# Kernel tuning notes

Hardware: AMD Instinct MI355X
Metric: run time of the kernel (lower is better)

Reference implementation:

```python
import jax, jax.numpy as jnp
import numpy as np

T, N, D, H = 128, 512, 1024, 1024
LN_EPS = 1e-5


def setup_inputs() -> dict:
    key = jax.random.key(0)
    ks = jax.random.split(key, 6)
    x = jax.random.normal(ks[0], (T * N, D), jnp.float32)
    hxs = jax.random.normal(ks[1], (N, 1, H), jnp.float32)
    # binary done-masks (float, mostly 1.0 = keep hidden state, 0.0 = episode reset)
    masks = (jax.random.uniform(ks[2], (T * N, 1)) < 0.95).astype(jnp.float32)
    s = 1.0 / np.sqrt(H)
    # PyTorch GRU packed gates, order (r, z, n): weight_ih_l0 [3H, D], weight_hh_l0 [3H, H]
    W_ih = jax.random.normal(ks[3], (3 * H, D), jnp.float32) * s
    W_hh = jax.random.normal(ks[4], (3 * H, H), jnp.float32) * s
    b_ih = jnp.zeros((3 * H,), jnp.float32)  # module inits biases to 0
    b_hh = jnp.zeros((3 * H,), jnp.float32)
    gamma = jnp.ones((H,), jnp.float32)
    beta = jnp.zeros((H,), jnp.float32)
    return dict(x=x, hxs=hxs, masks=masks, W_ih=W_ih, W_hh=W_hh,
                b_ih=b_ih, b_hh=b_hh, gamma=gamma, beta=beta)


def reference(x, hxs, masks, W_ih, W_hh, b_ih, b_hh, gamma, beta):
    TN = x.shape[0]
    Nn = hxs.shape[0]
    Tt = TN // Nn
    Hd = hxs.shape[-1]
    xs = x.reshape(Tt, Nn, -1)          # [T, N, D]
    m = masks.reshape(Tt, Nn)           # [T, N]
    # Chunk starts per source: t=0 plus every t>=1 where (masks[t] == 1).any().
    # At a chunk start the hidden state is multiplied by masks[t] (broadcast over layers);
    # a scan with a per-step conditional mask-multiply is exactly equivalent to the
    # torch loop over chunks.
    reset = jnp.concatenate([jnp.ones((1,), bool), jnp.any(m[1:] == 1.0, axis=-1)])
    # Batch the input projection across all T*N tokens (one big GEMM): [T, N, 3H]
    xp = jnp.einsum('tnd,gd->tng', xs, W_ih) + b_ih
    h0 = hxs[:, 0, :]                   # recurrent_N == 1 -> [N, H]

    def step(h, inp):
        xp_t, m_t, r_t = inp
        h = jnp.where(r_t, h * m_t[:, None], h)
        hp = h @ W_hh.T + b_hh          # [N, 3H]
        xr, xz, xn = jnp.split(xp_t, 3, axis=-1)
        hr, hz, hn = jnp.split(hp, 3, axis=-1)
        r = jax.nn.sigmoid(xr + hr)
        z = jax.nn.sigmoid(xz + hz)
        n = jnp.tanh(xn + r * hn)
        h_new = (1.0 - z) * n + z * h
        return h_new, h_new

    h_last, outs = jax.lax.scan(step, h0, (xp, m, reset))
    y = outs.reshape(Tt * Nn, Hd)
    # LayerNorm over last dim
    mu = y.mean(-1, keepdims=True)
    var = y.var(-1, keepdims=True)
    y = (y - mu) * jax.lax.rsqrt(var + LN_EPS) * gamma + beta
    return y, h_last[:, None, :]
```

## Files before the change

kernel.cpp:

```cpp
#include <hip/hip_runtime.h>

#define T_STEPS 128
#define N_B     512
#define D_IN    1024
#define H_DIM   1024
#define G_DIM   3072
#define M_ALL   (T_STEPS * N_B)
#define BAR_STRIDE 64

typedef short          s8v  __attribute__((ext_vector_type(8)));
typedef float          f4v  __attribute__((ext_vector_type(4)));
typedef unsigned short u4v  __attribute__((ext_vector_type(4)));

__device__ __forceinline__ unsigned short f2bf(float f) {
  union { float f; unsigned u; } v; v.f = f;
  unsigned r = v.u + 0x7FFFu + ((v.u >> 16) & 1u);
  return (unsigned short)(r >> 16);
}
__device__ __forceinline__ float bf2f(unsigned short h) {
  union { unsigned u; float f; } v; v.u = ((unsigned)h) << 16;
  return v.f;
}
__device__ __forceinline__ void async16(const void* g, void* l) {
  __builtin_amdgcn_global_load_lds(
      (const __attribute__((address_space(1))) unsigned*)g,
      (__attribute__((address_space(3))) unsigned*)l, 16, 0, 0);
}
__device__ __forceinline__ void async16_coh(const void* g, void* l) {
  __builtin_amdgcn_global_load_lds(
      (const __attribute__((address_space(1))) unsigned*)g,
      (__attribute__((address_space(3))) unsigned*)l, 16, 0, 17);
}
__device__ __forceinline__ void store_bf16_coh(unsigned short* p, unsigned short v) {
  unsigned v32 = v;
  asm volatile("global_store_short %0, %1, off sc0 sc1" :: "v"(p), "v"(v32) : "memory");
}
__device__ __forceinline__ float sigmoidf_(float x) { return 1.f / (1.f + __expf(-x)); }
__device__ __forceinline__ float tanhf_(float x)    { return 1.f - 2.f / (1.f + __expf(2.f * x)); }

__global__ void cvt_bf16(const float* __restrict__ in, unsigned short* __restrict__ out, long n4) {
  long i = (long)blockIdx.x * blockDim.x + threadIdx.x;
  long stride = (long)gridDim.x * blockDim.x;
  for (; i < n4; i += stride) {
    f4v v = *(const f4v*)(in + i * 4);
    u4v o;
    #pragma unroll
    for (int e = 0; e < 4; ++e) o[e] = f2bf(v[e]);
    *(u4v*)(out + i * 4) = o;
  }
}

__global__ void reset_kernel(const float* __restrict__ masks, int* __restrict__ reset) {
  const int t = blockIdx.x;
  __shared__ int flag;
  if (threadIdx.x == 0) flag = (t == 0) ? 1 : 0;
  __syncthreads();
  if (t > 0 && masks[(size_t)t * N_B + threadIdx.x] == 1.0f) flag = 1;
  __syncthreads();
  if (threadIdx.x == 0) reset[t] = flag;
}

__global__ __launch_bounds__(256) void gemm_xp(const unsigned short* __restrict__ A,
                                               const unsigned short* __restrict__ B,
                                               const float* __restrict__ bias,
                                               unsigned short* __restrict__ C) {
  const int m0 = blockIdx.y * 128, g0 = blockIdx.x * 128;
  const int tid = threadIdx.x, wv = tid >> 6, l = tid & 63;
  const int l15 = l & 15, l4 = l >> 4;
  const int wr = wv >> 1, wc = wv & 1;
  __shared__ unsigned short As[128 * 64], Bs[128 * 64];

  f4v zero4 = {0.f, 0.f, 0.f, 0.f};
  f4v acc[4][4];
  #pragma unroll
  for (int i = 0; i < 4; ++i)
    #pragma unroll
    for (int j = 0; j < 4; ++j) acc[i][j] = zero4;

  const int srow = l >> 3;
  const int selem = ((l & 7) ^ srow) * 8;
  const int swz_rd = (l15 & 7) << 4;

  for (int kt = 0; kt < 1024; kt += 64) {
    #pragma unroll
    for (int cc = 0; cc < 4; ++cc) {
      int s = wv * 4 + cc;
      int row = s * 8 + srow;
      async16(A + (size_t)(m0 + row) * 1024 + kt + selem, &As[s * 512]);
      async16(B + (size_t)(g0 + row) * 1024 + kt + selem, &Bs[s * 512]);
    }
    __syncthreads();
    #pragma unroll
    for (int ks = 0; ks < 2; ++ks) {
      s8v a[4], b[4];
      #pragma unroll
      for (int i = 0; i < 4; ++i) {
        int ra = wr * 64 + i * 16 + l15, rb = wc * 64 + i * 16 + l15;
        int cb = (ks * 64 + l4 * 16) ^ swz_rd;
        a[i] = *(const s8v*)((const char*)As + ra * 128 + cb);
        b[i] = *(const s8v*)((const char*)Bs + rb * 128 + cb);
      }
      #pragma unroll
      for (int i = 0; i < 4; ++i)
        #pragma unroll
        for (int j = 0; j < 4; ++j)
          acc[i][j] = __builtin_amdgcn_mfma_f32_16x16x32_bf16(a[i], b[j], acc[i][j], 0, 0, 0);
    }
    __syncthreads();
  }
  #pragma unroll
  for (int j = 0; j < 4; ++j) {
    int gcol = g0 + wc * 64 + j * 16 + l15;
    float bv = bias[gcol];
    #pragma unroll
    for (int i = 0; i < 4; ++i) {
      int mrow = m0 + wr * 64 + i * 16 + l4 * 4;
      u4v o;
      #pragma unroll
      for (int r = 0; r < 4; ++r) o[r] = f2bf(acc[i][j][r] + bv);
      *(u4v*)(C + (size_t)gcol * M_ALL + mrow) = o;
    }
  }
}

__global__ __launch_bounds__(256, 1) void rnn_all(
    const unsigned short* __restrict__ Whh,
    const unsigned short* __restrict__ xpT,
    const float* __restrict__ masks,
    const int* __restrict__ reset,
    const float* __restrict__ bhh,
    const float* __restrict__ hxs,
    unsigned short* hbuf,
    float* __restrict__ y,
    float* __restrict__ hlast,
    unsigned* bar) {
  const int bid = blockIdx.x;
  const int jt = bid & 31, nt = bid >> 5;
  const int j0 = jt * 32, n0 = nt * 64;
  const int tid = threadIdx.x, w = tid >> 6, l = tid & 63;
  const int l15 = l & 15, l4 = l >> 4;
  const int wn = w & 1, wj = w >> 1;
  const size_t NH = (size_t)N_B * H_DIM;

  __shared__ unsigned short Hs[3][64 * 128];
  __shared__ unsigned short Ws[3][96 * 128];
  __shared__ unsigned short xpl[3][32][64];

  const int lrow4 = l >> 4;
  const int lcb = (l & 15) * 16;
  const int swz_rd = (l15 & 7) << 4;

  const int jj = j0 + wj * 16 + l15;
  const float br = bhh[jj];
  const float bz = bhh[H_DIM + jj];
  const float bn = bhh[2 * H_DIM + jj];

  float hreg[2][4];
  #pragma unroll
  for (int i = 0; i < 2; ++i)
    #pragma unroll
    for (int r = 0; r < 4; ++r)
      hreg[i][r] = hxs[(size_t)(n0 + wn * 32 + i * 16 + l4 * 4 + r) * H_DIM + jj];

  f4v zero4 = {0.f, 0.f, 0.f, 0.f};
  s8v zer8 = {0, 0, 0, 0, 0, 0, 0, 0};

  auto stageH = [&](const unsigned short* hread, int buf, int kt) {
    #pragma unroll
    for (int q = 0; q < 4; ++q) {
      int rb = w * 16 + q * 4;
      int row = rb + lrow4;
      int cb = lcb ^ ((row & 7) << 4);
      async16_coh(hread + (size_t)(n0 + row) * H_DIM + kt * 128 + (cb >> 1),
                  &Hs[buf][rb * 128]);
    }
  };
  auto stageW = [&](int buf, int kt) {
    #pragma unroll
    for (int q = 0; q < 6; ++q) {
      int rb = w * 24 + q * 4;
      int row = rb + lrow4;
      int gate = row >> 5, jjl = row & 31;
      int cb = lcb ^ ((row & 7) << 4);
      async16(Whh + ((size_t)gate * H_DIM + j0 + jjl) * H_DIM + kt * 128 + (cb >> 1),
              &Ws[buf][rb * 128]);
    }
  };
  auto stageXP = [&](int t) {
    const int jl = w * 8 + (l >> 3);
    const int nelem = ((l & 7) ^ (l >> 3)) * 8;
    #pragma unroll
    for (int g3 = 0; g3 < 3; ++g3)
      async16(xpT + (size_t)(g3 * H_DIM + j0 + jl) * M_ALL + (size_t)t * N_B + n0 + nelem,
              &xpl[g3][w * 8][0]);
  };

  int rst = reset[0];
  bool zo[2];
  float mreg[2][4];
  #pragma unroll
  for (int i = 0; i < 2; ++i) {
    float mv = masks[(size_t)0 * N_B + n0 + wn * 32 + i * 16 + l15];
    zo[i] = rst && (mv == 0.0f);
  }
  #pragma unroll
  for (int i = 0; i < 2; ++i)
    #pragma unroll
    for (int r = 0; r < 4; ++r)
      mreg[i][r] = masks[(size_t)0 * N_B + n0 + wn * 32 + i * 16 + l4 * 4 + r];
  stageW(0, 0); stageW(1, 1); stageW(2, 2);
  stageXP(0);

  for (int t = 0; t < T_STEPS; ++t) {
    const unsigned short* hread = hbuf + (size_t)(t & 1) * NH;
    unsigned short* hwrite = hbuf + (size_t)((t & 1) ^ 1) * NH;

    stageH(hread, 0, 0); stageH(hread, 1, 1); stageH(hread, 2, 2);

    f4v acc[2][3];
    #pragma unroll
    for (int i = 0; i < 2; ++i)
      #pragma unroll
      for (int g3 = 0; g3 < 3; ++g3) acc[i][g3] = zero4;

#define KT_BODY(KT, VM, DO_STAGE)                                              \
    {                                                                          \
      asm volatile("s_waitcnt vmcnt(" #VM ")" ::: "memory");                   \
      __builtin_amdgcn_s_barrier();                                            \
      __builtin_amdgcn_sched_barrier(0);                                       \
      if (DO_STAGE) { stageH(hread, (KT + 2) % 3, KT + 2); stageW((KT + 2) % 3, KT + 2); } \
      const char* hb = (const char*)&Hs[KT % 3][0];                            \
      const char* wb = (const char*)&Ws[KT % 3][0];                            \
      _Pragma("unroll")                                                        \
      for (int ks = 0; ks < 4; ++ks) {                                         \
        const int kbb = (ks * 64 + l4 * 16) ^ swz_rd;                          \
        s8v a[2], b[3];                                                        \
        _Pragma("unroll")                                                      \
        for (int i = 0; i < 2; ++i) {                                          \
          a[i] = *(const s8v*)(hb + (wn * 32 + i * 16 + l15) * 256 + kbb);     \
          if (zo[i]) a[i] = zer8;                                              \
        }                                                                      \
        _Pragma("unroll")                                                      \
        for (int g3 = 0; g3 < 3; ++g3)                                         \
          b[g3] = *(const s8v*)(wb + (g3 * 32 + wj * 16 + l15) * 256 + kbb);   \
        _Pragma("unroll")                                                      \
        for (int i = 0; i < 2; ++i)                                            \
          _Pragma("unroll")                                                    \
          for (int g3 = 0; g3 < 3; ++g3)                                       \
            acc[i][g3] = __builtin_amdgcn_mfma_f32_16x16x32_bf16(a[i], b[g3],  \
                                                                acc[i][g3], 0, 0, 0); \
      }                                                                        \
    }

    KT_BODY(0, 8,  false)
    KT_BODY(1, 4,  true)
    KT_BODY(2, 10, true)
    KT_BODY(3, 10, true)
    KT_BODY(4, 10, true)
    KT_BODY(5, 10, true)
    KT_BODY(6, 10, false)
    KT_BODY(7, 0,  false)
#undef KT_BODY

    #pragma unroll
    for (int i = 0; i < 2; ++i) {
      #pragma unroll
      for (int r = 0; r < 4; ++r) {
        const int n = n0 + wn * 32 + i * 16 + l4 * 4 + r;
        const int nl = wn * 32 + i * 16 + l4 * 4 + r;
        const int jl = wj * 16 + l15;
        float hprev = hreg[i][r];
        if (rst && mreg[i][r] == 0.0f) hprev = 0.0f;
        const float hr = acc[i][0][r] + br;
        const float hz = acc[i][1][r] + bz;
        const float hn = acc[i][2][r] + bn;
        const char* xb = (const char*)&xpl[0][0][0];
        const int nb = (nl * 2) ^ ((jl & 7) << 4);
        const float xr = bf2f(*(const unsigned short*)(xb + 0 * 4096 + jl * 128 + nb));
        const float xz = bf2f(*(const unsigned short*)(xb + 1 * 4096 + jl * 128 + nb));
        const float xn = bf2f(*(const unsigned short*)(xb + 2 * 4096 + jl * 128 + nb));
        const float rg = sigmoidf_(xr + hr);
        const float zg = sigmoidf_(xz + hz);
        const float ng = tanhf_(xn + rg * hn);
        const float hnew = (1.f - zg) * ng + zg * hprev;
        hreg[i][r] = hnew;
        const size_t gidx = (size_t)n * H_DIM + jj;
        y[(size_t)t * NH + gidx] = hnew;
        store_bf16_coh(hwrite + gidx, f2bf(hnew));
        if (t == T_STEPS - 1) hlast[gidx] = hnew;
      }
    }

    __syncthreads();

    int rstN = 0;
    bool zoN[2] = {false, false};
    float mregN[2][4];
    if (t + 1 < T_STEPS) {
      rstN = reset[t + 1];
      #pragma unroll
      for (int i = 0; i < 2; ++i) {
        float mv = masks[(size_t)(t + 1) * N_B + n0 + wn * 32 + i * 16 + l15];
        zoN[i] = rstN && (mv == 0.0f);
      }
      #pragma unroll
      for (int i = 0; i < 2; ++i)
        #pragma unroll
        for (int r = 0; r < 4; ++r)
          mregN[i][r] = masks[(size_t)(t + 1) * N_B + n0 + wn * 32 + i * 16 + l4 * 4 + r];
      stageW(0, 0); stageW(1, 1); stageW(2, 2);
      stageXP(t + 1);
    }

    if (tid == 0) {
      __hip_atomic_fetch_add(&bar[nt * BAR_STRIDE], 1u, __ATOMIC_RELAXED, __HIP_MEMORY_SCOPE_AGENT);
      const unsigned tgt = 32u * (unsigned)(t + 1);
      while (__hip_atomic_load(&bar[nt * BAR_STRIDE], __ATOMIC_RELAXED, __HIP_MEMORY_SCOPE_AGENT) < tgt)
        __builtin_amdgcn_s_sleep(1);
    }
    __builtin_amdgcn_s_barrier();
    __builtin_amdgcn_sched_barrier(0);

    rst = rstN;
    #pragma unroll
    for (int i = 0; i < 2; ++i) {
      zo[i] = zoN[i];
      #pragma unroll
      for (int r = 0; r < 4; ++r) mreg[i][r] = mregN[i][r];
    }
  }
}

__global__ __launch_bounds__(256) void ln_kernel(float* __restrict__ y,
                                                 const float* __restrict__ gamma,
                                                 const float* __restrict__ beta) {
  const size_t row = blockIdx.x;
  float* p = y + row * (size_t)H_DIM;
  const int tid = threadIdx.x;
  f4v v = *(const f4v*)(p + tid * 4);
  float s = v[0] + v[1] + v[2] + v[3];
  float q = v[0] * v[0] + v[1] * v[1] + v[2] * v[2] + v[3] * v[3];
  #pragma unroll
  for (int off = 32; off > 0; off >>= 1) {
    s += __shfl_down(s, off);
    q += __shfl_down(q, off);
  }
  __shared__ float sb[8];
  const int wid = tid >> 6, lid = tid & 63;
  if (lid == 0) { sb[wid] = s; sb[4 + wid] = q; }
  __syncthreads();
  float S = sb[0] + sb[1] + sb[2] + sb[3];
  float Q = sb[4] + sb[5] + sb[6] + sb[7];
  float mean = S * (1.f / H_DIM);
  float var = Q * (1.f / H_DIM) - mean * mean;
  float inv = rsqrtf(var + 1e-5f);
  f4v g4 = *(const f4v*)(gamma + tid * 4);
  f4v b4 = *(const f4v*)(beta + tid * 4);
  f4v o;
  #pragma unroll
  for (int e = 0; e < 4; ++e) o[e] = (v[e] - mean) * inv * g4[e] + b4[e];
  *(f4v*)(p + tid * 4) = o;
}

extern "C" void kernel_launch(void* const* d_in, const int* in_sizes, int n_in,
                              void* d_out, int out_size, void* d_ws, size_t ws_size,
                              hipStream_t stream) {
  const float* x     = (const float*)d_in[0];
  const float* hxs   = (const float*)d_in[1];
  const float* masks = (const float*)d_in[2];
  const float* W_ih  = (const float*)d_in[3];
  const float* W_hh  = (const float*)d_in[4];
  const float* b_ih  = (const float*)d_in[5];
  const float* b_hh  = (const float*)d_in[6];
  const float* gamma = (const float*)d_in[7];
  const float* beta  = (const float*)d_in[8];
  float* y = (float*)d_out;
  float* hlast = y + (size_t)T_STEPS * N_B * H_DIM;

  char* ws = (char*)d_ws;
  unsigned short* Wih_bf = (unsigned short*)ws;  ws += (size_t)G_DIM * D_IN * 2;
  unsigned short* Whh_bf = (unsigned short*)ws;  ws += (size_t)G_DIM * H_DIM * 2;
  unsigned short* xc_bf  = (unsigned short*)ws;  ws += (size_t)M_ALL * D_IN * 2;
  unsigned short* xpT_bf = (unsigned short*)ws;  ws += (size_t)G_DIM * M_ALL * 2;
  unsigned short* hbuf   = (unsigned short*)ws;  ws += (size_t)2 * N_B * H_DIM * 2;
  unsigned* bars         = (unsigned*)ws;        ws += 8 * BAR_STRIDE * sizeof(unsigned);
  int* reset             = (int*)ws;             ws += 512;

  hipMemsetAsync(bars, 0, 8 * BAR_STRIDE * sizeof(unsigned), stream);
  cvt_bf16<<<1024, 256, 0, stream>>>(W_ih, Wih_bf, (long)G_DIM * D_IN / 4);
  cvt_bf16<<<1024, 256, 0, stream>>>(W_hh, Whh_bf, (long)G_DIM * H_DIM / 4);
  cvt_bf16<<<512, 256, 0, stream>>>(hxs, hbuf, (long)N_B * H_DIM / 4);
  reset_kernel<<<128, 512, 0, stream>>>(masks, reset);
  cvt_bf16<<<4096, 256, 0, stream>>>(x, xc_bf, (long)M_ALL * D_IN / 4);

  dim3 gg(G_DIM / 128, M_ALL / 128);
  gemm_xp<<<gg, 256, 0, stream>>>(xc_bf, Wih_bf, b_ih, xpT_bf);

  rnn_all<<<256, 256, 0, stream>>>(Whh_bf, xpT_bf, masks, reset, b_hh,
                                   hxs, hbuf, y, hlast, bars);

  ln_kernel<<<T_STEPS * N_B, 256, 0, stream>>>(y, gamma, beta);
}
```

Before: 2.266 ms.

## Rewrite input-projection GEMM with 256x128 tiles, triple-buffered async loads, XCD-aware grid

Replaces the input-projection GEMM with a 512-thread kernel using 256x128 output tiles. K-slices are staged through a three-deep LDS ring buffer, with explicit vmcnt waits so global loads overlap MFMA work. Blocks are remapped so each XCD handles a contiguous band of M rows, which should improve L2 reuse. Priority hints are raised around the MFMA section. The cost is higher LDS use (about 144KB) and one block per CU, which leaves less occupancy to hide latency.

```diff
diff --git a/kernel.cpp b/kernel.cpp
--- a/kernel.cpp
+++ b/kernel.cpp
@@ -60,64 +60,92 @@
   if (threadIdx.x == 0) reset[t] = flag;
 }
 
-__global__ __launch_bounds__(256) void gemm_xp(const unsigned short* __restrict__ A,
-                                               const unsigned short* __restrict__ B,
-                                               const float* __restrict__ bias,
-                                               unsigned short* __restrict__ C) {
-  const int m0 = blockIdx.y * 128, g0 = blockIdx.x * 128;
-  const int tid = threadIdx.x, wv = tid >> 6, l = tid & 63;
+__global__ __launch_bounds__(512, 1) void gemm_xp2(const unsigned short* __restrict__ A,
+                                                   const unsigned short* __restrict__ B,
+                                                   const float* __restrict__ bias,
+                                                   unsigned short* __restrict__ C) {
+  const int p = blockIdx.x;
+  const int xcd = p & 7, r = p >> 3;
+  const int by = xcd * 32 + r / 24;
+  const int bx = r % 24;
+  const int m0 = by * 256, n0 = bx * 128;
+  const int tid = threadIdx.x, wid = tid >> 6, l = tid & 63;
   const int l15 = l & 15, l4 = l >> 4;
-  const int wr = wv >> 1, wc = wv & 1;
-  __shared__ unsigned short As[128 * 64], Bs[128 * 64];
-
-  f4v zero4 = {0.f, 0.f, 0.f, 0.f};
-  f4v acc[4][4];
-  #pragma unroll
-  for (int i = 0; i < 4; ++i)
-    #pragma unroll
-    for (int j = 0; j < 4; ++j) acc[i][j] = zero4;
+  const int wm = wid >> 2, wn = wid & 3;
+
+  __shared__ unsigned short As[3][256 * 64];
+  __shared__ unsigned short Bs[3][128 * 64];
 
   const int srow = l >> 3;
   const int selem = ((l & 7) ^ srow) * 8;
   const int swz_rd = (l15 & 7) << 4;
 
-  for (int kt = 0; kt < 1024; kt += 64) {
-    #pragma unroll
-    for (int cc = 0; cc < 4; ++cc) {
-      int s = wv * 4 + cc;
+  f4v zero4 = {0.f, 0.f, 0.f, 0.f};
+  f4v acc[8][2];
+  #pragma unroll
+  for (int i = 0; i < 8; ++i)
+    #pragma unroll
+    for (int j = 0; j < 2; ++j) acc[i][j] = zero4;
+
+  auto stage = [&](int buf, int kt) {
+    #pragma unroll
+    for (int c = 0; c < 4; ++c) {
+      int s = wid * 4 + c;
       int row = s * 8 + srow;
-      async16(A + (size_t)(m0 + row) * 1024 + kt + selem, &As[s * 512]);
-      async16(B + (size_t)(g0 + row) * 1024 + kt + selem, &Bs[s * 512]);
-    }
-    __syncthreads();
+      async16(A + (size_t)(m0 + row) * 1024 + kt * 64 + selem, &As[buf][s * 512]);
+    }
+    #pragma unroll
+    for (int c = 0; c < 2; ++c) {
+      int s = wid * 2 + c;
+      int row = s * 8 + srow;
+      async16(B + (size_t)(n0 + row) * 1024 + kt * 64 + selem, &Bs[buf][s * 512]);
+    }
+  };
+
+  stage(0, 0); stage(1, 1); stage(2, 2);
+
+  for (int kt = 0; kt < 16; ++kt) {
+    if (kt < 14)       asm volatile("s_waitcnt vmcnt(12)" ::: "memory");
+    else if (kt == 14) asm volatile("s_waitcnt vmcnt(6)"  ::: "memory");
+    else               asm volatile("s_waitcnt vmcnt(0)"  ::: "memory");
+    __builtin_amdgcn_s_barrier();
+    __builtin_amdgcn_sched_barrier(0);
+    const int buf = kt % 3;
+    const char* ab = (const char*)&As[buf][0];
+    const char* bb = (const char*)&Bs[buf][0];
+    __builtin_amdgcn_s_setprio(1);
     #pragma unroll
     for (int ks = 0; ks < 2; ++ks) {
-      s8v a[4], b[4];
-      #pragma unroll
-      for (int i = 0; i < 4; ++i) {
-        int ra = wr * 64 + i * 16 + l15, rb = wc * 64 + i * 16 + l15;
-        int cb = (ks * 64 + l4 * 16) ^ swz_rd;
-        a[i] = *(const s8v*)((const char*)As + ra * 128 + cb);
-        b[i] = *(const s8v*)((const char*)Bs + rb * 128 + cb);
-      }
-      #pragma unroll
-      for (int i = 0; i < 4; ++i)
+      const int kbb = (ks * 64 + l4 * 16) ^ swz_rd;
+      s8v a[8], b[2];
+      #pragma unroll
+      for (int i = 0; i < 8; ++i)
+        a[i] = *(const s8v*)(ab + (wm * 128 + i * 16 + l15) * 128 + kbb);
+      #pragma unroll
+      for (int j = 0; j < 2; ++j)
+        b[j] = *(const s8v*)(bb + (wn * 32 + j * 16 + l15) * 128 + kbb);
+      #pragma unroll
+      for (int i = 0; i < 8; ++i)
         #pragma unroll
-        for (int j = 0; j < 4; ++j)
+        for (int j = 0; j < 2; ++j)
           acc[i][j] = __builtin_amdgcn_mfma_f32_16x16x32_bf16(a[i], b[j], acc[i][j], 0, 0, 0);
     }
-    __syncthreads();
-  }
-  #pragma unroll
-  for (int j = 0; j < 4; ++j) {
-    int gcol = g0 + wc * 64 + j * 16 + l15;
+    __builtin_amdgcn_s_setprio(0);
+    __builtin_amdgcn_s_barrier();
+    __builtin_amdgcn_sched_barrier(0);
+    if (kt + 3 < 16) stage(buf, kt + 3);
+  }
+
+  #pragma unroll
+  for (int j = 0; j < 2; ++j) {
+    int gcol = n0 + wn * 32 + j * 16 + l15;
     float bv = bias[gcol];
     #pragma unroll
-    for (int i = 0; i < 4; ++i) {
-      int mrow = m0 + wr * 64 + i * 16 + l4 * 4;
+    for (int i = 0; i < 8; ++i) {
+      int mrow = m0 + wm * 128 + i * 16 + l4 * 4;
       u4v o;
       #pragma unroll
-      for (int r = 0; r < 4; ++r) o[r] = f2bf(acc[i][j][r] + bv);
+      for (int rr = 0; rr < 4; ++rr) o[rr] = f2bf(acc[i][j][rr] + bv);
       *(u4v*)(C + (size_t)gcol * M_ALL + mrow) = o;
     }
   }
@@ -393,8 +421,7 @@
   reset_kernel<<<128, 512, 0, stream>>>(masks, reset);
   cvt_bf16<<<4096, 256, 0, stream>>>(x, xc_bf, (long)M_ALL * D_IN / 4);
 
-  dim3 gg(G_DIM / 128, M_ALL / 128);
-  gemm_xp<<<gg, 256, 0, stream>>>(xc_bf, Wih_bf, b_ih, xpT_bf);
+  gemm_xp2<<<6144, 512, 0, stream>>>(xc_bf, Wih_bf, b_ih, xpT_bf);
 
   rnn_all<<<256, 256, 0, stream>>>(Whh_bf, xpT_bf, masks, reset, b_hh,
                                    hxs, hbuf, y, hlast, bars);
```

Result: slower. 2.538 ms (+12.0%).
